# Performance work log

Hardware: AMD Instinct MI355X
Metric: run time of the kernel (lower is better)

Reference implementation:

```python
import jax, jax.numpy as jnp
import numpy as np

B, N, D, S = 16, 16384, 64, 7
H = 128                       # hidden_dim = max(dim, 128)
ITERS, MESH_ITERS, SH_ITERS = 3, 4, 5
MESH_LR = 1.0
EPS = 1e-8


def _ln(x, g, b, eps=1e-5):
    m = jnp.mean(x, -1, keepdims=True)
    v = jnp.mean((x - m) ** 2, -1, keepdims=True)
    return (x - m) * jax.lax.rsqrt(v + eps) * g + b


def _l2norm(x, eps=1e-12):
    n = jnp.sqrt(jnp.sum(x * x, -1, keepdims=True))
    return x / jnp.maximum(n, eps)


def _sinkhorn(C, log_a, log_b, u, v, n_iters):
    # log-domain Sinkhorn; C: (B, N, S), marginals a:(B,N) sum=S, b:(B,S) sum=S
    p = -C
    def body(carry, _):
        u, v = carry
        u = log_a - jax.nn.logsumexp(p + v[:, None, :], axis=2)
        v = log_b - jax.nn.logsumexp(p + u[:, :, None], axis=1)
        return (u, v), None
    (u, v), _ = jax.lax.scan(body, (u, v), None, length=n_iters)
    attn = jnp.exp(p + u[:, :, None] + v[:, None, :])
    return attn, u, v


def _mesh(C, log_a, log_b):
    # minimize entropy of sinkhorn: gradient descent on C w.r.t. plan entropy,
    # warm-starting dual potentials (u, v) across MESH steps.
    u = jnp.zeros_like(log_a)
    v = jnp.zeros_like(log_b)
    for _ in range(MESH_ITERS):
        def ent(Cc, u=u, v=v):
            attn, uu, vv = _sinkhorn(Cc, log_a, log_b, u, v, SH_ITERS)
            # per-sample entropy summed (samples are independent)
            return -jnp.sum(attn * jnp.log(attn + EPS)), (uu, vv)
        g, (u, v) = jax.grad(ent, has_aux=True)(C)
        C = C - MESH_LR * g
    return C, u, v


def setup_inputs() -> dict:
    key = jax.random.key(0)
    ks = jax.random.split(key, 26)
    f = lambda k, sh: jax.random.normal(k, sh, dtype=jnp.float32)
    s = np.float32(1.0 / np.sqrt(D))
    sh = np.float32(1.0 / np.sqrt(H))
    return {
        'inputs': f(ks[0], (B, N, D)),
        'slot_noise': f(ks[1], (B, S, D)),
        'slots_mu': f(ks[2], (1, 1, D)) * s,
        'slots_sigma': jax.random.uniform(ks[3], (1, 1, D), dtype=jnp.float32),
        'Wq': f(ks[4], (D, D)) * s,
        'Wk': f(ks[5], (D, D)) * s,
        'Wv': f(ks[6], (D, D)) * s,
        'gru_w_ih': f(ks[7], (3 * D, D)) * s,
        'gru_w_hh': f(ks[8], (3 * D, D)) * s,
        'gru_b_ih': f(ks[9], (3 * D,)) * s,
        'gru_b_hh': f(ks[10], (3 * D,)) * s,
        'fc1_w': f(ks[11], (H, D)) * s,
        'fc1_b': f(ks[12], (H,)) * s,
        'fc2_w': f(ks[13], (D, H)) * sh,
        'fc2_b': f(ks[14], (D,)) * sh,
        'ln_in_g': jnp.ones((D,), jnp.float32),
        'ln_in_b': jnp.zeros((D,), jnp.float32),
        'ln_sl_g': jnp.ones((D,), jnp.float32),
        'ln_sl_b': jnp.zeros((D,), jnp.float32),
        'ln_ff_g': jnp.ones((D,), jnp.float32),
        'ln_ff_b': jnp.zeros((D,), jnp.float32),
        'wi_w': f(ks[15], (1, D)) * s,
        'wi_b': jnp.zeros((1,), jnp.float32),
        'ws_w': f(ks[16], (1, D)) * s,
        'ws_b': jnp.zeros((1,), jnp.float32),
    }


def reference(inputs, slot_noise, slots_mu, slots_sigma, Wq, Wk, Wv,
              gru_w_ih, gru_w_hh, gru_b_ih, gru_b_hh,
              fc1_w, fc1_b, fc2_w, fc2_b,
              ln_in_g, ln_in_b, ln_sl_g, ln_sl_b, ln_ff_g, ln_ff_b,
              wi_w, wi_b, ws_w, ws_b):
    n_s = slot_noise.shape[1]
    # reparameterized Normal(mu, |sigma|+eps) sample
    slots = slots_mu + (jnp.abs(slots_sigma) + EPS) * slot_noise      # (B,S,D)
    x = _ln(inputs, ln_in_g, ln_in_b)                                  # (B,N,D)
    k = x @ Wk.T
    val = x @ Wv.T
    a = jax.nn.softmax((x @ wi_w.T + wi_b)[..., 0], axis=-1) * n_s     # (B,N)
    log_a = jnp.log(a)
    kn = _l2norm(k)
    for _ in range(ITERS):
        slots_prev = slots
        sn = _ln(slots, ln_sl_g, ln_sl_b)
        bm = jax.nn.softmax((sn @ ws_w.T + ws_b)[..., 0], axis=-1) * n_s  # (B,S)
        log_b = jnp.log(bm)
        q = sn @ Wq.T
        C = 1.0 - jnp.einsum('bnd,bsd->bns', kn, _l2norm(q))            # cosine distance
        C, u, v = _mesh(C, log_a, log_b)
        attn, _, _ = _sinkhorn(C, log_a, log_b, u, v, SH_ITERS)         # (B,N,S)
        attn_t = jnp.swapaxes(attn, 1, 2)                               # (B,S,N)
        updates = jnp.einsum('bsn,bnd->bsd', attn_t, val)
        # GRUCell (torch gate order: r, z, n)
        gx = updates @ gru_w_ih.T + gru_b_ih
        gh = slots_prev @ gru_w_hh.T + gru_b_hh
        xr, xz, xn = jnp.split(gx, 3, axis=-1)
        hr, hz, hn = jnp.split(gh, 3, axis=-1)
        r = jax.nn.sigmoid(xr + hr)
        z = jax.nn.sigmoid(xz + hz)
        n = jnp.tanh(xn + r * hn)
        slots = (1.0 - z) * n + z * slots_prev
        ff = _ln(slots, ln_ff_g, ln_ff_b)
        slots = slots + jax.nn.relu(ff @ fc1_w.T + fc1_b) @ fc2_w.T + fc2_b
    return slots, attn_t
```

## Files before the change

### kernel.cpp

```cpp
#include <hip/hip_runtime.h>

typedef unsigned int u32;
typedef unsigned short u16;
typedef unsigned long long u64;

#define NT 16384
#define LN7 1.9459101090932196f
#define ZWORDS 118784

__device__ __forceinline__ u32 f2bf(float f){
  u32 u = __float_as_uint(f);
  return (u + 0x7fffu + ((u >> 16) & 1u)) >> 16;
}
__device__ __forceinline__ float bflo(u32 v){ return __uint_as_float(v << 16); }

__global__ __launch_bounds__(1024) void k_zero(u64* p){
  int i = blockIdx.x * 1024 + threadIdx.x;
  if (i < ZWORDS) p[i] = 0ull;
}

__device__ __forceinline__ void st_dev(u64* p, u64 v){
  asm volatile("global_store_dwordx2 %0, %1, off sc0 sc1" :: "v"(p), "v"(v) : "memory");
}
__device__ __forceinline__ void ld2_dev(const u64* p0, const u64* p1, u64& a, u64& b){
  asm volatile("global_load_dwordx2 %0, %2, off sc0 sc1\n\t"
               "global_load_dwordx2 %1, %3, off sc0 sc1\n\t"
               "s_waitcnt vmcnt(0)"
               : "=&v"(a), "=&v"(b) : "v"(p0), "v"(p1) : "memory");
}
__device__ __forceinline__ u64 ld_issue(const u64* p){
  u64 v;
  asm volatile("global_load_dwordx2 %0, %1, off sc0 sc1" : "=v"(v) : "v"(p));
  return v;
}

__global__ __launch_bounds__(1024) void k_pre(
    const float* __restrict__ inp,
    const float* __restrict__ Wk, const float* __restrict__ Wv,
    const float* __restrict__ lning, const float* __restrict__ lninb,
    const float* __restrict__ wiw, const float* __restrict__ wib,
    u16* __restrict__ knb, u16* __restrict__ valb,
    float* __restrict__ lgA, float* __restrict__ rnA,
    float* __restrict__ lsePart)
{
  const int tid = threadIdx.x, blk = blockIdx.x;
  const int batch = blk >> 7, chunk = blk & 127;
  const size_t growbase = ((size_t)batch << 14) + ((size_t)chunk << 7);

  __shared__ float Xs[64*132];
  __shared__ float Ws[64*132];
  __shared__ float red[16][2];

  {
    const int r = tid >> 3, p = tid & 7, base8 = p << 3;
    const size_t row = growbase + r;
    float x8[8];
    const float4* xp = (const float4*)(inp + row*64 + base8);
    float4 a = xp[0], b = xp[1];
    x8[0]=a.x; x8[1]=a.y; x8[2]=a.z; x8[3]=a.w;
    x8[4]=b.x; x8[5]=b.y; x8[6]=b.z; x8[7]=b.w;
    float s1 = 0.f;
    #pragma unroll
    for (int i = 0; i < 8; ++i) s1 += x8[i];
    #pragma unroll
    for (int off = 1; off < 8; off <<= 1) s1 += __shfl_xor(s1, off, 64);
    const float mean = s1 * (1.f/64.f);
    float s2 = 0.f;
    #pragma unroll
    for (int i = 0; i < 8; ++i){ float d = x8[i]-mean; s2 += d*d; }
    #pragma unroll
    for (int off = 1; off < 8; off <<= 1) s2 += __shfl_xor(s2, off, 64);
    const float rstd = rsqrtf(s2*(1.f/64.f) + 1e-5f);
    float lgp = 0.f;
    #pragma unroll
    for (int i = 0; i < 8; ++i){
      float xv = (x8[i]-mean)*rstd*lning[base8+i] + lninb[base8+i];
      lgp += xv*wiw[base8+i];
      Xs[(base8+i)*132 + r] = xv;
    }
    #pragma unroll
    for (int off = 1; off < 8; off <<= 1) lgp += __shfl_xor(lgp, off, 64);
    const float lg = lgp + wib[0];
    if (p == 0) lgA[row] = lg;
    float m = (p == 0) ? lg : -3.4e38f;
    float s = (p == 0) ? 1.f : 0.f;
    #pragma unroll
    for (int off = 1; off < 64; off <<= 1){
      float om = __shfl_xor(m, off, 64);
      float os = __shfl_xor(s, off, 64);
      float nm = fmaxf(m, om);
      s = s*__expf(m-nm) + os*__expf(om-nm);
      m = nm;
    }
    if ((tid & 63) == 0){ red[tid>>6][0] = m; red[tid>>6][1] = s; }
  }

  {
    const int c = tid >> 3, k0 = (tid & 7) << 3;
    const float* src = (c < 64) ? (Wk + c*64 + k0) : (Wv + (size_t)(c-64)*64 + k0);
    float4 w0 = *(const float4*)src;
    float4 w1 = *(const float4*)(src + 4);
    Ws[(k0+0)*132 + c] = w0.x; Ws[(k0+1)*132 + c] = w0.y;
    Ws[(k0+2)*132 + c] = w0.z; Ws[(k0+3)*132 + c] = w0.w;
    Ws[(k0+4)*132 + c] = w1.x; Ws[(k0+5)*132 + c] = w1.y;
    Ws[(k0+6)*132 + c] = w1.z; Ws[(k0+7)*132 + c] = w1.w;
  }
  __syncthreads();
  if (tid == 0){
    float M = red[0][0];
    for (int w = 1; w < 16; ++w) M = fmaxf(M, red[w][0]);
    float S = 0.f;
    for (int w = 0; w < 16; ++w) S += __expf(red[w][0]-M)*red[w][1];
    lsePart[blk*2+0] = M;
    lsePart[blk*2+1] = S;
  }

  const int tr = tid >> 5, tc = tid & 31;
  float acc[4][4] = {{0.f,0.f,0.f,0.f},{0.f,0.f,0.f,0.f},
                     {0.f,0.f,0.f,0.f},{0.f,0.f,0.f,0.f}};
  #pragma unroll 4
  for (int kk = 0; kk < 64; ++kk){
    float4 a4 = *(const float4*)&Xs[kk*132 + 4*tr];
    float4 b4 = *(const float4*)&Ws[kk*132 + 4*tc];
    float av[4] = {a4.x, a4.y, a4.z, a4.w};
    float bv[4] = {b4.x, b4.y, b4.z, b4.w};
    #pragma unroll
    for (int i = 0; i < 4; ++i)
      #pragma unroll
      for (int j = 0; j < 4; ++j) acc[i][j] += av[i]*bv[j];
  }

  if (tc < 16){
    float ssq[4];
    #pragma unroll
    for (int i = 0; i < 4; ++i)
      ssq[i] = acc[i][0]*acc[i][0] + acc[i][1]*acc[i][1]
             + acc[i][2]*acc[i][2] + acc[i][3]*acc[i][3];
    #pragma unroll
    for (int off = 1; off < 16; off <<= 1)
      #pragma unroll
      for (int i = 0; i < 4; ++i) ssq[i] += __shfl_xor(ssq[i], off, 64);
    if (tc == 0){
      #pragma unroll
      for (int i = 0; i < 4; ++i)
        rnA[growbase + 4*tr + i] = 1.f/fmaxf(sqrtf(ssq[i]), 1e-12f);
    }
    #pragma unroll
    for (int i = 0; i < 4; ++i){
      u32 lo = f2bf(acc[i][0]) | (f2bf(acc[i][1]) << 16);
      u32 hi = f2bf(acc[i][2]) | (f2bf(acc[i][3]) << 16);
      *(uint2*)(knb + (growbase + 4*tr + i)*64 + 4*tc) = make_uint2(lo, hi);
    }
  } else {
    const int tcv = tc - 16;
    #pragma unroll
    for (int i = 0; i < 4; ++i){
      u32 lo = f2bf(acc[i][0]) | (f2bf(acc[i][1]) << 16);
      u32 hi = f2bf(acc[i][2]) | (f2bf(acc[i][3]) << 16);
      *(uint2*)(valb + (growbase + 4*tr + i)*64 + 4*tcv) = make_uint2(lo, hi);
    }
  }
}

__global__ __launch_bounds__(1024) void k_mesh(
    const float* __restrict__ noise, const float* __restrict__ mu,
    const float* __restrict__ sigma, const float* __restrict__ Wq,
    const float* __restrict__ gwih, const float* __restrict__ gwhh,
    const float* __restrict__ gbih, const float* __restrict__ gbhh,
    const float* __restrict__ fc1w, const float* __restrict__ fc1b,
    const float* __restrict__ fc2w, const float* __restrict__ fc2b,
    const float* __restrict__ lnslg, const float* __restrict__ lnslb,
    const float* __restrict__ lnffg, const float* __restrict__ lnffb,
    const float* __restrict__ wsw, const float* __restrict__ wsb,
    const u16* __restrict__ knb, const u16* __restrict__ valb,
    const float* __restrict__ lgA, const float* __restrict__ rnA,
    const float* __restrict__ lsePart,
    u64* Tp, u64* upT, float* out)
{
  const int tid = threadIdx.x;
  const int blk = blockIdx.x;
  const int batch = (blk & 7) | ((blk >> 7) << 3);
  const int party = (blk >> 3) & 15;
  const int bp    = (batch << 4) | party;
  const int rbase = party << 10;

  __shared__ float Sl[7][64], Qn[7][64], Qt[7][64], Sst[7][64];
  __shared__ float Gx[7][192], Gh[7][192], H1[7][128];
  __shared__ float uacc[16][7][64];
  __shared__ float red[16][8];
  __shared__ float vhL[6][8], logb[8], evT5L[8];
  __shared__ float polW[128];
  __shared__ float ecL[1024*9];
  __shared__ float pbL[1024*9];
  __shared__ float aRL[1024];
  __shared__ float rse5L[1024];
  __shared__ float sS[2];

  float* ab = out + 7168 + (size_t)batch * 7 * NT;

  u32 bstep = 0;
  int tbuf = 0;

  if (tid == 0){
    const float* lp = lsePart + batch*256;
    float M = lp[0];
    for (int w = 1; w < 128; ++w) M = fmaxf(M, lp[2*w]);
    float S = 0.f;
    for (int w = 0; w < 128; ++w) S += __expf(lp[2*w] - M) * lp[2*w + 1];
    sS[0] = M + __logf(S);
  }
  __syncthreads();
  const float LSE = sS[0];
  const size_t gr = ((size_t)batch << 14) | (size_t)(rbase | tid);
  aRL[tid] = __expf(lgA[gr] - LSE + LN7);

  for (int it = 0; it < 3; ++it){
    if (tid < 448){
      float sl;
      if (it == 0){
        const int d = tid & 63;
        sl = mu[d] + (fabsf(sigma[d]) + 1e-8f) * noise[batch*448 + tid];
      } else sl = Sst[tid>>6][tid&63];
      Sl[tid>>6][tid&63] = sl;
    }
    if (tid < 8) vhL[5][tid] = 0.f;
    __syncthreads();
    if (tid < 7){
      float m2 = 0.f;
      for (int d = 0; d < 64; ++d) m2 += Sl[tid][d];
      m2 *= (1.f/64.f);
      float v2 = 0.f;
      for (int d = 0; d < 64; ++d){ float dd = Sl[tid][d]-m2; v2 += dd*dd; }
      v2 *= (1.f/64.f);
      float rs2 = rsqrtf(v2 + 1e-5f);
      float lgq = wsb[0];
      for (int d = 0; d < 64; ++d){
        float s = (Sl[tid][d]-m2)*rs2*lnslg[d] + lnslb[d];
        Qt[tid][d] = s;
        lgq += s*wsw[d];
      }
      red[0][tid] = lgq;
    }
    __syncthreads();
    if (tid == 0){
      float mx = red[0][0];
      for (int s = 1; s < 7; ++s) mx = fmaxf(mx, red[0][s]);
      float sm = 0.f;
      for (int s = 0; s < 7; ++s) sm += __expf(red[0][s]-mx);
      float lse = mx + __logf(sm);
      for (int s = 0; s < 7; ++s) logb[s] = red[0][s] - lse + LN7;
    }
    __syncthreads();
    if (tid < 448){
      const int s = tid >> 6, d = tid & 63;
      const float* wr = Wq + d*64;
      float acc2 = 0.f;
      #pragma unroll
      for (int dd = 0; dd < 64; ++dd) acc2 += Qt[s][dd]*wr[dd];
      Sl[s][d] = acc2;
    }
    __syncthreads();
    if (tid < 7){
      float sq = 0.f;
      for (int d = 0; d < 64; ++d) sq += Sl[tid][d]*Sl[tid][d];
      red[1][tid] = 1.f/fmaxf(sqrtf(sq), 1e-12f);
    }
    __syncthreads();
    if (tid < 448) Qn[tid>>6][tid&63] = Sl[tid>>6][tid&63]*red[1][tid>>6];
    __syncthreads();

    {
      float acc[7] = {0.f,0.f,0.f,0.f,0.f,0.f,0.f};
      const uint4* kr = (const uint4*)(knb + gr*64);
      #pragma unroll
      for (int q8 = 0; q8 < 8; ++q8){
        uint4 kv = kr[q8];
        float f0=bflo(kv.x), f1=__uint_as_float(kv.x & 0xffff0000u);
        float f2=bflo(kv.y), f3=__uint_as_float(kv.y & 0xffff0000u);
        float f4=bflo(kv.z), f5=__uint_as_float(kv.z & 0xffff0000u);
        float f6=bflo(kv.w), f7=__uint_as_float(kv.w & 0xffff0000u);
        const int d0 = q8*8;
        #pragma unroll
        for (int s = 0; s < 7; ++s){
          const float4 qa = *(const float4*)&Qn[s][d0];
          const float4 qb = *(const float4*)&Qn[s][d0+4];
          acc[s] += f0*qa.x + f1*qa.y + f2*qa.z + f3*qa.w
                  + f4*qb.x + f5*qb.y + f6*qb.z + f7*qb.w;
        }
      }
      const float rn_ = rnA[gr];
      #pragma unroll
      for (int s = 0; s < 7; ++s)
        ecL[tid*9+s] = __expf(-(1.f - rn_*acc[s]));
    }
    __syncthreads();

    if (tid < 64){
      const int lane = tid;
      float logb7[7];
      #pragma unroll
      for (int s = 0; s < 7; ++s) logb7[s] = logb[s];

      auto sync7 = [&](float (&part)[7], float (&T7)[7]){
        #pragma unroll
        for (int off = 32; off > 0; off >>= 1)
          #pragma unroll
          for (int s = 0; s < 7; ++s) part[s] += __shfl_xor(part[s], off, 64);
        ++bstep;
        float pv = part[0];
        pv = (lane==1)?part[1]:pv; pv = (lane==2)?part[2]:pv;
        pv = (lane==3)?part[3]:pv; pv = (lane==4)?part[4]:pv;
        pv = (lane==5)?part[5]:pv; pv = (lane==6)?part[6]:pv;
        if (lane < 7)
          st_dev(&Tp[(tbuf<<11) + bp*8 + lane],
                 ((u64)bstep << 32) | (u64)__float_as_uint(pv));
        const u64* base = &Tp[(tbuf<<11) + (size_t)(batch << 4)*8];
        const bool isPad = ((lane & 7) == 7);
        u64 v0, v1; bool ok;
        do {
          ld2_dev(base + lane, base + 64 + lane, v0, v1);
          ok = isPad || (((u32)(v0>>32) == bstep) && ((u32)(v1>>32) == bstep));
        } while (!__all(ok));
        polW[lane]      = __uint_as_float((u32)v0);
        polW[64 + lane] = __uint_as_float((u32)v1);
        #pragma unroll
        for (int s = 0; s < 7; ++s){
          float T = 0.f;
          #pragma unroll
          for (int w = 0; w < 16; ++w) T += polW[w*8+s];
          T7[s] = T;
        }
        tbuf ^= 1;
      };

      float ev[7], vwv[7], rtv[7];
      #pragma unroll 1
      for (int m = 0; m < 5; ++m){
        float mxp[6];
        {
          float v5[7];
          #pragma unroll
          for (int s = 0; s < 7; ++s) v5[s] = vhL[5][s];
          float mxn = v5[0];
          #pragma unroll
          for (int s = 1; s < 7; ++s) mxn = fmaxf(mxn, v5[s]);
          if (lane == 0){
            #pragma unroll
            for (int s = 0; s < 7; ++s) vhL[0][s] = v5[s];
          }
          mxp[1] = mxn;
          #pragma unroll
          for (int s = 0; s < 7; ++s) ev[s] = __expf(v5[s] - mxn);
        }
        #pragma unroll
        for (int t = 1; t <= 5; ++t){
          float t7[7] = {0.f,0.f,0.f,0.f,0.f,0.f,0.f};
          #pragma unroll 2
          for (int rr = 0; rr < 16; ++rr){
            const int row = (rr << 6) | lane;
            float e[7];
            #pragma unroll
            for (int s = 0; s < 7; ++s) e[s] = ecL[row*9+s];
            const float aRr = aRL[row];
            float se = e[0]*ev[0];
            #pragma unroll
            for (int s = 1; s < 7; ++s) se += e[s]*ev[s];
            const float rse = 1.f/se;
            if (t == 5) rse5L[row] = rse;
            const float w = aRr*rse;
            #pragma unroll
            for (int s = 0; s < 7; ++s) t7[s] += w*e[s];
          }
          float T7[7];
          sync7(t7, T7);
          float vht[7];
          #pragma unroll
          for (int s = 0; s < 7; ++s) vht[s] = logb7[s] + mxp[t] - __logf(T7[s]);
          if (lane == 0){
            #pragma unroll
            for (int s = 0; s < 7; ++s) vhL[t][s] = vht[s];
          }
          if (t < 5){
            float mxn = vht[0];
            #pragma unroll
            for (int s = 1; s < 7; ++s) mxn = fmaxf(mxn, vht[s]);
            mxp[t+1] = mxn;
            #pragma unroll
            for (int s = 0; s < 7; ++s) ev[s] = __expf(vht[s] - mxn);
          } else {
            #pragma unroll
            for (int s = 0; s < 7; ++s) ev[s] = __expf(vht[s] - mxp[5]);
          }
        }
        if (m == 4) break;
        {
          float vh5r[7];
          #pragma unroll
          for (int s = 0; s < 7; ++s) vh5r[s] = vhL[5][s];
          const float mx5 = mxp[5];
          float gs[7] = {0.f,0.f,0.f,0.f,0.f,0.f,0.f};
          #pragma unroll 2
          for (int rr = 0; rr < 16; ++rr){
            const int row = (rr << 6) | lane;
            float e[7];
            #pragma unroll
            for (int s = 0; s < 7; ++s) e[s] = ecL[row*9+s];
            const float aRr = aRL[row];
            const float r5 = rse5L[row];
            const float q = aRr*r5;
            const float basel = __logf(aRr) - mx5 + __logf(r5);
            #pragma unroll
            for (int s = 0; s < 7; ++s){
              float at = q * e[s] * ev[s];
              float lat = basel + vh5r[s] + __logf(e[s]);
              float G = -at * (lat + 1.f);
              pbL[row*9+s] = G;
              gs[s] += G;
            }
          }
          float T7[7];
          sync7(gs, T7);
          #pragma unroll
          for (int s = 0; s < 7; ++s){
            vwv[s] = T7[s] * __expf(vh5r[s] - logb7[s] - mxp[5]);
            rtv[s] = __expf(vhL[4][s] - mxp[5]);
          }
        }
        #pragma unroll
        for (int t = 5; t >= 1; --t){
          float evt[7];
          #pragma unroll
          for (int s = 0; s < 7; ++s) evt[s] = __expf(vhL[t-1][s] - mxp[t]);
          float ra[7] = {0.f,0.f,0.f,0.f,0.f,0.f,0.f};
          #pragma unroll 2
          for (int rr = 0; rr < 16; ++rr){
            const int row = (rr << 6) | lane;
            float e[7], pb[7];
            #pragma unroll
            for (int s = 0; s < 7; ++s) e[s] = ecL[row*9+s];
            #pragma unroll
            for (int s = 0; s < 7; ++s) pb[s] = pbL[row*9+s];
            const float aRr = aRL[row];
            float se = e[0]*evt[0];
            #pragma unroll
            for (int s = 1; s < 7; ++s) se += e[s]*evt[s];
            const float rse = 1.f/se;
            float ub = 0.f;
            if (t == 5){
              #pragma unroll
              for (int s = 0; s < 7; ++s) ub += pb[s];
            }
            float s1 = e[0]*vwv[0];
            #pragma unroll
            for (int s = 1; s < 7; ++s) s1 += e[s]*vwv[s];
            ub -= aRr * rse * s1;
            const float u2 = ub * rse;
            const float ar_ = aRr * rse;
            #pragma unroll
            for (int s = 0; s < 7; ++s){
              float er = e[s] * rtv[s];
              ra[s] += u2 * er;
              pb[s] -= ar_ * vwv[s] * e[s] + u2 * er;
            }
            if (t > 1){
              #pragma unroll
              for (int s = 0; s < 7; ++s) pbL[row*9+s] = pb[s];
            } else {
              #pragma unroll
              for (int s = 0; s < 7; ++s) ecL[row*9+s] = e[s] * __expf(-pb[s]);
            }
          }
          if (t > 1){
            float T7[7];
            sync7(ra, T7);
            #pragma unroll
            for (int s = 0; s < 7; ++s){
              vwv[s] = -T7[s] * __expf(vhL[t-1][s] - logb7[s] - mxp[t-1]);
              rtv[s] = __expf(vhL[t-2][s] - mxp[t-1]);
            }
          }
        }
      }
      if (lane == 0){
        #pragma unroll
        for (int s = 0; s < 7; ++s) evT5L[s] = ev[s];
      }
    }
    __syncthreads();

    {
      const int n = rbase | tid;
      const float wq = aRL[tid] * rse5L[tid];
      #pragma unroll
      for (int s = 0; s < 7; ++s) ab[s*NT + n] = wq * ecL[tid*9+s] * evT5L[s];
    }
    __syncthreads();

    {
      const int w = tid >> 6, d = tid & 63;
      const int nb = rbase + (w << 6);
      float acc[7] = {0.f,0.f,0.f,0.f,0.f,0.f,0.f};
      const u16* vbp = valb + (((size_t)batch << 14) + (size_t)nb)*64 + d;
      #pragma unroll 1
      for (int i = 0; i < 64; i += 4){
        float4 a4[7];
        #pragma unroll
        for (int s = 0; s < 7; ++s) a4[s] = *(const float4*)(ab + s*NT + nb + i);
        #pragma unroll
        for (int j = 0; j < 4; ++j){
          float vv = bflo((u32)vbp[(size_t)(i+j)*64]);
          #pragma unroll
          for (int s = 0; s < 7; ++s) acc[s] += ((const float*)&a4[s])[j] * vv;
        }
      }
      #pragma unroll
      for (int s = 0; s < 7; ++s) uacc[w][s][d] = acc[s];
    }
    __syncthreads();

    {
      const u32 utag = (u32)(it + 1);
      if (tid < 448){
        float u_ = 0.f;
        #pragma unroll
        for (int w = 0; w < 16; ++w) u_ += uacc[w][tid >> 6][tid & 63];
        st_dev(&upT[(size_t)bp*448 + tid],
               ((u64)utag << 32) | (u64)__float_as_uint(u_));
        const u64* base = &upT[(size_t)(batch << 4)*448 + tid];
        u64 vv[16];
        bool ok;
        do{
          #pragma unroll
          for (int p = 0; p < 16; ++p) vv[p] = ld_issue(base + p*448);
          asm volatile("s_waitcnt vmcnt(0)"
            : "+v"(vv[0]),"+v"(vv[1]),"+v"(vv[2]),"+v"(vv[3]),
              "+v"(vv[4]),"+v"(vv[5]),"+v"(vv[6]),"+v"(vv[7]),
              "+v"(vv[8]),"+v"(vv[9]),"+v"(vv[10]),"+v"(vv[11]),
              "+v"(vv[12]),"+v"(vv[13]),"+v"(vv[14]),"+v"(vv[15])
            :: "memory");
          ok = true;
          #pragma unroll
          for (int p = 0; p < 16; ++p) ok = ok && ((u32)(vv[p] >> 32) == utag);
        } while (!__all(ok));
        float u_t = 0.f;
        #pragma unroll
        for (int p = 0; p < 16; ++p) u_t += __uint_as_float((u32)vv[p]);
        Sl[tid>>6][tid&63] = u_t;
        float sp;
        if (it == 0){
          const int d = tid & 63;
          sp = mu[d] + (fabsf(sigma[d]) + 1e-8f) * noise[batch*448 + tid];
        } else sp = Sst[tid>>6][tid&63];
        Qt[tid>>6][tid&63] = sp;
      }
    }
    __syncthreads();

    for (int o = tid; o < 2688; o += 1024){
      const int sl = o / 384, oo = o - sl*384;
      if (oo < 192){
        const float* wr = gwih + oo*64;
        float acc2 = gbih[oo];
        #pragma unroll
        for (int dd = 0; dd < 64; ++dd) acc2 += Sl[sl][dd]*wr[dd];
        Gx[sl][oo] = acc2;
      } else {
        const int o2 = oo - 192;
        const float* wr = gwhh + o2*64;
        float acc2 = gbhh[o2];
        #pragma unroll
        for (int dd = 0; dd < 64; ++dd) acc2 += Qt[sl][dd]*wr[dd];
        Gh[sl][o2] = acc2;
      }
    }
    __syncthreads();
    if (tid < 448){
      const int s = tid >> 6, d = tid & 63;
      float r = 1.f/(1.f + __expf(-(Gx[s][d] + Gh[s][d])));
      float z = 1.f/(1.f + __expf(-(Gx[s][64+d] + Gh[s][64+d])));
      float nn2 = tanhf(Gx[s][128+d] + r*Gh[s][128+d]);
      Qn[s][d] = (1.f - z)*nn2 + z*Qt[s][d];
    }
    __syncthreads();
    if (tid < 7){
      float m2 = 0.f;
      for (int d = 0; d < 64; ++d) m2 += Qn[tid][d];
      m2 *= (1.f/64.f);
      float v2 = 0.f;
      for (int d = 0; d < 64; ++d){ float dd = Qn[tid][d]-m2; v2 += dd*dd; }
      v2 *= (1.f/64.f);
      float rs2 = rsqrtf(v2 + 1e-5f);
      for (int d = 0; d < 64; ++d)
        Sl[tid][d] = (Qn[tid][d]-m2)*rs2*lnffg[d] + lnffb[d];
    }
    __syncthreads();
    if (tid < 896){
      const int s = tid >> 7, h = tid & 127;
      const float* f1 = fc1w + h*64;
      float acc2 = fc1b[h];
      #pragma unroll
      for (int d = 0; d < 64; ++d) acc2 += Sl[s][d]*f1[d];
      H1[s][h] = fmaxf(acc2, 0.f);
    }
    __syncthreads();
    if (tid < 448){
      const int s = tid >> 6, d = tid & 63;
      const float* f2 = fc2w + d*128;
      float o2 = fc2b[d];
      #pragma unroll
      for (int h = 0; h < 128; ++h) o2 += H1[s][h]*f2[h];
      float res = Qn[s][d] + o2;
      Sst[s][d] = res;
      if (it == 2 && party == 0) out[batch*448 + tid] = res;
    }
    __syncthreads();
  }
}

extern "C" void kernel_launch(void* const* d_in, const int* in_sizes, int n_in,
                              void* d_out, int out_size, void* d_ws, size_t ws_size,
                              hipStream_t stream)
{
  const float* inp   = (const float*)d_in[0];
  const float* noise = (const float*)d_in[1];
  const float* mu    = (const float*)d_in[2];
  const float* sigma = (const float*)d_in[3];
  const float* Wq    = (const float*)d_in[4];
  const float* Wk    = (const float*)d_in[5];
  const float* Wv    = (const float*)d_in[6];
  const float* gwih  = (const float*)d_in[7];
  const float* gwhh  = (const float*)d_in[8];
  const float* gbih  = (const float*)d_in[9];
  const float* gbhh  = (const float*)d_in[10];
  const float* fc1w  = (const float*)d_in[11];
  const float* fc1b  = (const float*)d_in[12];
  const float* fc2w  = (const float*)d_in[13];
  const float* fc2b  = (const float*)d_in[14];
  const float* lning = (const float*)d_in[15];
  const float* lninb = (const float*)d_in[16];
  const float* lnslg = (const float*)d_in[17];
  const float* lnslb = (const float*)d_in[18];
  const float* lnffg = (const float*)d_in[19];
  const float* lnffb = (const float*)d_in[20];
  const float* wiw   = (const float*)d_in[21];
  const float* wib   = (const float*)d_in[22];
  const float* wsw   = (const float*)d_in[23];
  const float* wsb   = (const float*)d_in[24];

  char* w = (char*)d_ws;
  u16*   knb     = (u16*)(w);
  u16*   valb    = (u16*)(w + 33554432);
  float* lgA     = (float*)(w + 67108864);
  float* rnA     = (float*)(w + 68157440);
  float* lsePart = (float*)(w + 69206016);
  u64*   Tp      = (u64*)(w + 69222400);
  u64*   upT     = (u64*)(w + 69255168);

  k_zero<<<116, 1024, 0, stream>>>(Tp);
  k_pre<<<2048, 1024, 0, stream>>>(inp, Wk, Wv, lning, lninb, wiw, wib,
                                   knb, valb, lgA, rnA, lsePart);
  k_mesh<<<256, 1024, 0, stream>>>(noise, mu, sigma, Wq,
                                   gwih, gwhh, gbih, gbhh,
                                   fc1w, fc1b, fc2w, fc2b,
                                   lnslg, lnslb, lnffg, lnffb, wsw, wsb,
                                   knb, valb, lgA, rnA, lsePart,
                                   Tp, upT, (float*)d_out);
  (void)in_sizes; (void)n_in; (void)out_size; (void)ws_size;
}
```

Before: 1.210 ms.

## Use XCC-local L2 atomic polling for inter-block barrier when group shares XCC

```diff
diff --git a/kernel.cpp b/kernel.cpp
--- a/kernel.cpp
+++ b/kernel.cpp
@@ -6,7 +6,7 @@
 
 #define NT 16384
 #define LN7 1.9459101090932196f
-#define ZWORDS 118784
+#define ZWORDS 123136
 
 __device__ __forceinline__ u32 f2bf(float f){
   u32 u = __float_as_uint(f);
@@ -21,6 +21,12 @@
 
 __device__ __forceinline__ void st_dev(u64* p, u64 v){
   asm volatile("global_store_dwordx2 %0, %1, off sc0 sc1" :: "v"(p), "v"(v) : "memory");
+}
+__device__ __forceinline__ u64 ld_dev(const u64* p){
+  u64 v;
+  asm volatile("global_load_dwordx2 %0, %1, off sc0 sc1\n\ts_waitcnt vmcnt(0)"
+               : "=v"(v) : "v"(p) : "memory");
+  return v;
 }
 __device__ __forceinline__ void ld2_dev(const u64* p0, const u64* p1, u64& a, u64& b){
   asm volatile("global_load_dwordx2 %0, %2, off sc0 sc1\n\t"
@@ -32,6 +38,15 @@
   u64 v;
   asm volatile("global_load_dwordx2 %0, %1, off sc0 sc1" : "=v"(v) : "v"(p));
   return v;
+}
+__device__ __forceinline__ void st_l2(u64* p, u64 v){
+  asm volatile("global_store_dwordx2 %0, %1, off sc0" :: "v"(p), "v"(v) : "memory");
+}
+__device__ __forceinline__ void atom2_or0(u64* p0, u64* p1, u64& a, u64& b){
+  asm volatile("global_atomic_or_x2 %0, %2, %4, off sc0\n\t"
+               "global_atomic_or_x2 %1, %3, %4, off sc0\n\t"
+               "s_waitcnt vmcnt(0)"
+               : "=&v"(a), "=&v"(b) : "v"(p0), "v"(p1), "v"(0ull) : "memory");
 }
 
 __global__ __launch_bounds__(1024) void k_pre(
@@ -94,7 +109,6 @@
     }
     if ((tid & 63) == 0){ red[tid>>6][0] = m; red[tid>>6][1] = s; }
   }
-
   {
     const int c = tid >> 3, k0 = (tid & 7) << 3;
     const float* src = (c < 64) ? (Wk + c*64 + k0) : (Wv + (size_t)(c-64)*64 + k0);
@@ -129,7 +143,6 @@
       #pragma unroll
       for (int j = 0; j < 4; ++j) acc[i][j] += av[i]*bv[j];
   }
-
   if (tc < 16){
     float ssq[4];
     #pragma unroll
@@ -175,7 +188,7 @@
     const u16* __restrict__ knb, const u16* __restrict__ valb,
     const float* __restrict__ lgA, const float* __restrict__ rnA,
     const float* __restrict__ lsePart,
-    u64* Tp, u64* upT, float* out)
+    u64* Tp, u64* Tpf, u64* hs, u64* upT, float* out)
 {
   const int tid = threadIdx.x;
   const int blk = blockIdx.x;
@@ -195,13 +208,20 @@
   __shared__ float aRL[1024];
   __shared__ float rse5L[1024];
   __shared__ float sS[2];
+  __shared__ int sfast;
 
   float* ab = out + 7168 + (size_t)batch * 7 * NT;
 
   u32 bstep = 0;
   int tbuf = 0;
-
-  if (tid == 0){
+  int fastTries = 0, failcnt = 0;
+
+  u32 xcc;
+  asm volatile("s_getreg_b32 %0, hwreg(HW_REG_XCC_ID)" : "=s"(xcc));
+  xcc &= 0xffu;
+  if (tid == 0) st_dev(&hs[bp], (0xC0FFEEull << 32) | (u64)xcc);
+
+  if (tid == 1){
     const float* lp = lsePart + batch*256;
     float M = lp[0];
     for (int w = 1; w < 128; ++w) M = fmaxf(M, lp[2*w]);
@@ -209,7 +229,20 @@
     for (int w = 0; w < 128; ++w) S += __expf(lp[2*w] - M) * lp[2*w + 1];
     sS[0] = M + __logf(S);
   }
+  if (tid < 64){
+    u64 v = 0;
+    bool ok;
+    const u64* src = &hs[(batch << 4) + (tid & 15)];
+    do {
+      if (tid < 16) v = ld_dev(src);
+      ok = (tid >= 16) || ((u32)(v >> 32) == 0xC0FFEEu);
+    } while (!__all(ok));
+    int same = (tid >= 16) || (((u32)v & 0xffu) == xcc);
+    int all16 = __all(same);
+    if (tid == 0) sfast = all16;
+  }
   __syncthreads();
+  fastTries = (sfast != 0) ? 48 : 0;
   const float LSE = sS[0];
   const size_t gr = ((size_t)batch << 14) | (size_t)(rbase | tid);
   aRL[tid] = __expf(lgA[gr] - LSE + LN7);
@@ -311,16 +344,28 @@
         pv = (lane==1)?part[1]:pv; pv = (lane==2)?part[2]:pv;
         pv = (lane==3)?part[3]:pv; pv = (lane==4)?part[4]:pv;
         pv = (lane==5)?part[5]:pv; pv = (lane==6)?part[6]:pv;
-        if (lane < 7)
-          st_dev(&Tp[(tbuf<<11) + bp*8 + lane],
-                 ((u64)bstep << 32) | (u64)__float_as_uint(pv));
-        const u64* base = &Tp[(tbuf<<11) + (size_t)(batch << 4)*8];
+        if (lane < 7){
+          u64 word = ((u64)bstep << 32) | (u64)__float_as_uint(pv);
+          st_l2 (&Tpf[(tbuf<<11) + bp*8 + lane], word);
+          st_dev(&Tp [(tbuf<<11) + bp*8 + lane], word);
+        }
+        u64* baseF = &Tpf[(tbuf<<11) + (size_t)(batch << 4)*8];
+        const u64* baseD = &Tp[(tbuf<<11) + (size_t)(batch << 4)*8];
         const bool isPad = ((lane & 7) == 7);
-        u64 v0, v1; bool ok;
-        do {
-          ld2_dev(base + lane, base + 64 + lane, v0, v1);
-          ok = isPad || (((u32)(v0>>32) == bstep) && ((u32)(v1>>32) == bstep));
-        } while (!__all(ok));
+        u64 v0, v1; bool got = false;
+        for (int k = 0; k < fastTries; ++k){
+          atom2_or0(baseF + lane, baseF + 64 + lane, v0, v1);
+          bool ok = isPad || (((u32)(v0>>32) == bstep) && ((u32)(v1>>32) == bstep));
+          if (__all(ok)){ got = true; break; }
+        }
+        if (!got){
+          bool ok;
+          do {
+            ld2_dev(baseD + lane, baseD + 64 + lane, v0, v1);
+            ok = isPad || (((u32)(v0>>32) == bstep) && ((u32)(v1>>32) == bstep));
+          } while (!__all(ok));
+          if (fastTries){ if (++failcnt >= 2) fastTries = 0; }
+        }
         polW[lane]      = __uint_as_float((u32)v0);
         polW[64 + lane] = __uint_as_float((u32)v1);
         #pragma unroll
@@ -654,9 +699,11 @@
   float* rnA     = (float*)(w + 68157440);
   float* lsePart = (float*)(w + 69206016);
   u64*   Tp      = (u64*)(w + 69222400);
-  u64*   upT     = (u64*)(w + 69255168);
-
-  k_zero<<<116, 1024, 0, stream>>>(Tp);
+  u64*   Tpf     = (u64*)(w + 69255168);
+  u64*   hs      = (u64*)(w + 69287936);
+  u64*   upT     = (u64*)(w + 69289984);
+
+  k_zero<<<121, 1024, 0, stream>>>(Tp);
   k_pre<<<2048, 1024, 0, stream>>>(inp, Wk, Wv, lning, lninb, wiw, wib,
                                    knb, valb, lgA, rnA, lsePart);
   k_mesh<<<256, 1024, 0, stream>>>(noise, mu, sigma, Wq,
@@ -664,6 +711,6 @@
                                    fc1w, fc1b, fc2w, fc2b,
                                    lnslg, lnslb, lnffg, lnffb, wsw, wsb,
                                    knb, valb, lgA, rnA, lsePart,
-                                   Tp, upT, (float*)d_out);
+                                   Tp, Tpf, hs, upT, (float*)d_out);
   (void)in_sizes; (void)n_in; (void)out_size; (void)ws_size;
 }
```

Result: slower. 1.247 ms (+3.1%).

## Route cross-block reduction through a leader block that publishes aggregated totals

Applied to the files above, without the earlier changes.

```diff
diff --git a/kernel.cpp b/kernel.cpp
--- a/kernel.cpp
+++ b/kernel.cpp
@@ -6,7 +6,7 @@
 
 #define NT 16384
 #define LN7 1.9459101090932196f
-#define ZWORDS 118784
+#define ZWORDS 119040
 
 __device__ __forceinline__ u32 f2bf(float f){
   u32 u = __float_as_uint(f);
@@ -21,6 +21,12 @@
 
 __device__ __forceinline__ void st_dev(u64* p, u64 v){
   asm volatile("global_store_dwordx2 %0, %1, off sc0 sc1" :: "v"(p), "v"(v) : "memory");
+}
+__device__ __forceinline__ u64 ld_dev(const u64* p){
+  u64 v;
+  asm volatile("global_load_dwordx2 %0, %1, off sc0 sc1\n\ts_waitcnt vmcnt(0)"
+               : "=v"(v) : "v"(p) : "memory");
+  return v;
 }
 __device__ __forceinline__ void ld2_dev(const u64* p0, const u64* p1, u64& a, u64& b){
   asm volatile("global_load_dwordx2 %0, %2, off sc0 sc1\n\t"
@@ -94,7 +100,6 @@
     }
     if ((tid & 63) == 0){ red[tid>>6][0] = m; red[tid>>6][1] = s; }
   }
-
   {
     const int c = tid >> 3, k0 = (tid & 7) << 3;
     const float* src = (c < 64) ? (Wk + c*64 + k0) : (Wv + (size_t)(c-64)*64 + k0);
@@ -129,7 +134,6 @@
       #pragma unroll
       for (int j = 0; j < 4; ++j) acc[i][j] += av[i]*bv[j];
   }
-
   if (tc < 16){
     float ssq[4];
     #pragma unroll
@@ -175,7 +179,7 @@
     const u16* __restrict__ knb, const u16* __restrict__ valb,
     const float* __restrict__ lgA, const float* __restrict__ rnA,
     const float* __restrict__ lsePart,
-    u64* Tp, u64* upT, float* out)
+    u64* Tp, u64* Agg, u64* upT, float* out)
 {
   const int tid = threadIdx.x;
   const int blk = blockIdx.x;
@@ -314,21 +318,40 @@
         if (lane < 7)
           st_dev(&Tp[(tbuf<<11) + bp*8 + lane],
                  ((u64)bstep << 32) | (u64)__float_as_uint(pv));
-        const u64* base = &Tp[(tbuf<<11) + (size_t)(batch << 4)*8];
-        const bool isPad = ((lane & 7) == 7);
-        u64 v0, v1; bool ok;
-        do {
-          ld2_dev(base + lane, base + 64 + lane, v0, v1);
-          ok = isPad || (((u32)(v0>>32) == bstep) && ((u32)(v1>>32) == bstep));
-        } while (!__all(ok));
-        polW[lane]      = __uint_as_float((u32)v0);
-        polW[64 + lane] = __uint_as_float((u32)v1);
-        #pragma unroll
-        for (int s = 0; s < 7; ++s){
-          float T = 0.f;
-          #pragma unroll
-          for (int w = 0; w < 16; ++w) T += polW[w*8+s];
-          T7[s] = T;
+        if (party == 0){
+          const u64* baseD = &Tp[(tbuf<<11) + (size_t)(batch << 4)*8];
+          const bool isPad = ((lane & 7) == 7);
+          const int j = isPad ? (lane & 56) : lane;
+          u64 v0, v1; bool ok;
+          do {
+            ld2_dev(baseD + j, baseD + 64 + j, v0, v1);
+            ok = isPad || (((u32)(v0>>32) == bstep) && ((u32)(v1>>32) == bstep));
+          } while (!__all(ok));
+          polW[lane]      = __uint_as_float((u32)v0);
+          polW[64 + lane] = __uint_as_float((u32)v1);
+          #pragma unroll
+          for (int s = 0; s < 7; ++s){
+            float T = 0.f;
+            #pragma unroll
+            for (int w = 0; w < 16; ++w) T += polW[w*8+s];
+            T7[s] = T;
+          }
+          float tv = T7[0];
+          tv = (lane==1)?T7[1]:tv; tv = (lane==2)?T7[2]:tv;
+          tv = (lane==3)?T7[3]:tv; tv = (lane==4)?T7[4]:tv;
+          tv = (lane==5)?T7[5]:tv; tv = (lane==6)?T7[6]:tv;
+          if (lane < 7)
+            st_dev(&Agg[(tbuf<<7) + batch*8 + lane],
+                   ((u64)bstep << 32) | (u64)__float_as_uint(tv));
+        } else {
+          if (lane < 7){
+            const u64* asrc = &Agg[(tbuf<<7) + batch*8 + lane];
+            u64 v;
+            do { v = ld_dev(asrc); } while (!__all((u32)(v >> 32) == bstep));
+            polW[lane] = __uint_as_float((u32)v);
+          }
+          #pragma unroll
+          for (int s = 0; s < 7; ++s) T7[s] = polW[s];
         }
         tbuf ^= 1;
       };
@@ -654,9 +677,10 @@
   float* rnA     = (float*)(w + 68157440);
   float* lsePart = (float*)(w + 69206016);
   u64*   Tp      = (u64*)(w + 69222400);
-  u64*   upT     = (u64*)(w + 69255168);
-
-  k_zero<<<116, 1024, 0, stream>>>(Tp);
+  u64*   Agg     = (u64*)(w + 69255168);
+  u64*   upT     = (u64*)(w + 69257216);
+
+  k_zero<<<117, 1024, 0, stream>>>(Tp);
   k_pre<<<2048, 1024, 0, stream>>>(inp, Wk, Wv, lning, lninb, wiw, wib,
                                    knb, valb, lgA, rnA, lsePart);
   k_mesh<<<256, 1024, 0, stream>>>(noise, mu, sigma, Wq,
@@ -664,6 +688,6 @@
                                    fc1w, fc1b, fc2w, fc2b,
                                    lnslg, lnslb, lnffg, lnffb, wsw, wsb,
                                    knb, valb, lgA, rnA, lsePart,
-                                   Tp, upT, (float*)d_out);
+                                   Tp, Agg, upT, (float*)d_out);
   (void)in_sizes; (void)n_in; (void)out_size; (void)ws_size;
 }
```

Measured after the change: 1.369 ms. 1.13x slower.
